# Kernel optimization log

Hardware: AMD Instinct MI355X
Metric: run time of the kernel (lower is better)

Reference implementation:

```python
import jax, jax.numpy as jnp
import numpy as np

N_NODES = 100000


def _sage_conv(x, src, dst, W_l, b_l, W_r):
    # mean-aggregate neighbor (source) features at target nodes
    gathered = x[src]                                   # [E, D]
    summed = jax.ops.segment_sum(gathered, dst, num_segments=N_NODES)  # [N, D]
    deg = jax.ops.segment_sum(jnp.ones((src.shape[0],), x.dtype), dst,
                              num_segments=N_NODES)     # [N]
    mean = summed / jnp.maximum(deg, 1.0)[:, None]      # zero stays zero for isolated nodes
    # PyG SAGEConv: lin_l(aggr) + lin_r(x); bias on lin_l only
    return mean @ W_l + b_l + x @ W_r


def setup_inputs() -> dict:
    key = jax.random.key(0)
    ks = jax.random.split(key, 9)
    x = jax.random.normal(ks[0], (N_NODES, 128), dtype=jnp.float32)
    edge_index = jax.random.randint(ks[1], (2, 1600000), 0, N_NODES, dtype=jnp.int64)
    s1 = 1.0 / np.sqrt(128.0)
    s2 = 1.0 / np.sqrt(32.0)
    return {
        "x": x,
        "edge_index": edge_index,
        "W1_l": jax.random.normal(ks[2], (128, 32), jnp.float32) * s1,
        "b1_l": jax.random.normal(ks[3], (32,), jnp.float32) * s1,
        "W1_r": jax.random.normal(ks[4], (128, 32), jnp.float32) * s1,
        "W2_l": jax.random.normal(ks[5], (32, 32), jnp.float32) * s2,
        "b2_l": jax.random.normal(ks[6], (32,), jnp.float32) * s2,
        "W2_r": jax.random.normal(ks[7], (32, 32), jnp.float32) * s2,
    }


def reference(x, edge_index, W1_l, b1_l, W1_r, W2_l, b2_l, W2_r):
    src, dst = edge_index[0], edge_index[1]
    h = _sage_conv(x, src, dst, W1_l, b1_l, W1_r)
    h = jax.nn.relu(h)
    # dropout is identity in eval mode
    h = _sage_conv(h, src, dst, W2_l, b2_l, W2_r)
    return jax.nn.relu(h)
```

## Files before the change

kernel.cpp:

```cpp
#include <hip/hip_runtime.h>


typedef _Float16 f16;
typedef _Float16 f16x2 __attribute__((ext_vector_type(2)));
typedef _Float16 f16x4 __attribute__((ext_vector_type(4)));
typedef _Float16 half8 __attribute__((ext_vector_type(8)));
typedef float f32x4 __attribute__((ext_vector_type(4)));

#define MAXBINS 2048
#define SHIFT 6
#define BINSZ 64
#define CAP 48
#define BSTR 52
#define GSC 256
#define BSC 512
#define SRC_BITS 17
#define SRC_MASK 0x1FFFFu
#define XSTRIDE 136


__global__ __launch_bounds__(BSC) void block_hist(const int* __restrict__ dst,
                                                  int* __restrict__ blockHist,
                                                  int E, int chunk) {
    __shared__ int sh[MAXBINS];
    for (int i = threadIdx.x; i < MAXBINS; i += BSC) sh[i] = 0;
    __syncthreads();
    int base = blockIdx.x * chunk;
    int end = base + chunk < E ? base + chunk : E;
    for (int e = base + threadIdx.x; e < end; e += BSC)
        atomicAdd(&sh[dst[e] >> SHIFT], 1);
    __syncthreads();
    for (int i = threadIdx.x; i < MAXBINS; i += BSC)
        blockHist[(size_t)blockIdx.x * MAXBINS + i] = sh[i];
}

__global__ __launch_bounds__(256) void col_scan(const int* __restrict__ blockHist,
                                                int* __restrict__ blockBaseRel,
                                                int* __restrict__ binTot) {
    const int wave = threadIdx.x >> 6;
    const int lane = threadIdx.x & 63;
    const int bin = blockIdx.x * 4 + wave;
    int carry = 0;
#pragma unroll
    for (int r = 0; r < GSC / 64; ++r) {
        int b = r * 64 + lane;
        int v = blockHist[(size_t)b * MAXBINS + bin];
        int inc = v;
#pragma unroll
        for (int off = 1; off < 64; off <<= 1) {
            int t = __shfl_up(inc, off, 64);
            if (lane >= off) inc += t;
        }
        blockBaseRel[(size_t)b * MAXBINS + bin] = carry + (inc - v);
        carry += __shfl(inc, 63, 64);
    }
    binTot[bin] = carry;
}

__global__ __launch_bounds__(1024) void scan_bins(const int* __restrict__ binTot,
                                                  int* __restrict__ binStart,
                                                  int* __restrict__ binCnt) {
    __shared__ int sh[1024];
    int t = threadIdx.x;
    int v0 = binTot[2 * t], v1 = binTot[2 * t + 1];
    sh[t] = v0 + v1;
    __syncthreads();
    for (int off = 1; off < 1024; off <<= 1) {
        int x = 0;
        if (t >= off) x = sh[t - off];
        __syncthreads();
        sh[t] += x;
        __syncthreads();
    }
    int excl = sh[t] - (v0 + v1);
    binStart[2 * t] = excl;
    binStart[2 * t + 1] = excl + v0;
    binCnt[2 * t] = v0;
    binCnt[2 * t + 1] = v1;
}

__global__ __launch_bounds__(BSC) void scatter_binned(const int* __restrict__ src,
                                                      const int* __restrict__ dst,
                                                      const int* __restrict__ blockBaseRel,
                                                      const int* __restrict__ binStart,
                                                      unsigned* __restrict__ pairs,
                                                      int E, int chunk) {
    __shared__ int cur[MAXBINS];
    for (int i = threadIdx.x; i < MAXBINS; i += BSC)
        cur[i] = blockBaseRel[(size_t)blockIdx.x * MAXBINS + i] + binStart[i];
    __syncthreads();
    int base = blockIdx.x * chunk;
    int end = base + chunk < E ? base + chunk : E;
    for (int e = base + threadIdx.x; e < end; e += BSC) {
        int s = src[e], d = dst[e];
        int slot = atomicAdd(&cur[d >> SHIFT], 1);
        pairs[slot] = ((unsigned)(d & (BINSZ - 1)) << SRC_BITS) | (unsigned)s;
    }
}


__global__ __launch_bounds__(256) void gemm_mfma(const float* __restrict__ x,
                                                 const float* __restrict__ Wl,
                                                 const float* __restrict__ Wr,
                                                 f16* __restrict__ yl,
                                                 float* __restrict__ yr,
                                                 int N) {
    __shared__ f16 sX[64 * XSTRIDE];
    __shared__ f16 sWT[64 * XSTRIDE];
    const int tid = threadIdx.x;
    const int row0 = blockIdx.x * 64;

    for (int i = tid; i < 64 * 32; i += 256) {
        int r = i >> 5, c4 = i & 31;
        int row = row0 + r;
        float4 v = make_float4(0.f, 0.f, 0.f, 0.f);
        if (row < N) v = *(const float4*)(x + (size_t)row * 128 + c4 * 4);
        f16* d = &sX[r * XSTRIDE + c4 * 4];
        d[0] = (f16)v.x; d[1] = (f16)v.y; d[2] = (f16)v.z; d[3] = (f16)v.w;
    }
    for (int i = tid; i < 64 * 128; i += 256) {
        int k = i >> 6, n = i & 63;
        float v = (n < 32) ? Wl[k * 32 + n] : Wr[k * 32 + (n - 32)];
        sWT[n * XSTRIDE + k] = (f16)v;
    }
    __syncthreads();

    const int w = tid >> 6;
    const int lane = tid & 63;
    const int l15 = lane & 15, quad = lane >> 4;
    f32x4 acc[4] = {};
#pragma unroll
    for (int kc = 0; kc < 4; ++kc) {
        half8 af = *(const half8*)&sX[(w * 16 + l15) * XSTRIDE + kc * 32 + quad * 8];
#pragma unroll
        for (int nt = 0; nt < 4; ++nt) {
            half8 bf = *(const half8*)&sWT[(nt * 16 + l15) * XSTRIDE + kc * 32 + quad * 8];
            acc[nt] = __builtin_amdgcn_mfma_f32_16x16x32_f16(af, bf, acc[nt], 0, 0, 0);
        }
    }
#pragma unroll
    for (int nt = 0; nt < 4; ++nt) {
        int c = nt * 16 + l15;
#pragma unroll
        for (int r = 0; r < 4; ++r) {
            int g = row0 + w * 16 + quad * 4 + r;
            if (c < 32) yl[(size_t)g * 32 + c] = (f16)acc[nt][r];
            else        yr[(size_t)g * 32 + (c - 32)] = acc[nt][r];
        }
    }
}


__global__ __launch_bounds__(256) void agg_l1(const unsigned* __restrict__ pairs,
                                              const int* __restrict__ binStart,
                                              const int* __restrict__ binCnt,
                                              const f16* __restrict__ yl,
                                              const float* __restrict__ yr,
                                              const float* __restrict__ b1,
                                              const float* __restrict__ W2l,
                                              const float* __restrict__ W2r,
                                              f16* __restrict__ zl,
                                              float* __restrict__ zr,
                                              int N) {
    __shared__ __align__(16) int sBucket[BINSZ * BSTR];
    __shared__ int sCnt[BINSZ];
    __shared__ __align__(16) float sW[2048];
    __shared__ __align__(16) float sB[32];
    const int tid = threadIdx.x;
    if (tid < BINSZ) sCnt[tid] = 0;
    if (tid < 32) sB[tid] = b1[tid];
    for (int i = tid; i < 2048; i += 256) sW[i] = (i < 1024) ? W2l[i] : W2r[i - 1024];
    __syncthreads();

    const int b = blockIdx.x;
    const int start = binStart[b];
    const int endE = start + binCnt[b];
    for (int e = start + tid; e < endE; e += 256) {
        unsigned pk = pairs[e];
        int local = pk >> SRC_BITS;
        int slot = atomicAdd(&sCnt[local], 1);
        if (slot < CAP) sBucket[local * BSTR + slot] = (int)(pk & SRC_MASK);
    }
    __syncthreads();

    if (tid < BINSZ) {
        int c = sCnt[tid];
        int m = c < CAP ? c : CAP;
        int mp = (m + 7) & ~7;
        for (int k = m; k < mp; ++k) sBucket[tid * BSTR + k] = N;
    }
    __syncthreads();

    const int node = tid >> 2;
    const int c8 = tid & 3;
    const int node0 = b << SHIFT;
    const int g = node0 + node;

    const int deg = sCnt[node];
    const int m = deg < CAP ? deg : CAP;
    const int q = (m + 7) >> 3;
    const int4* bk = (const int4*)&sBucket[node * BSTR];
    const f16* yb = yl + c8 * 8;

    float ax[8] = {0.f, 0.f, 0.f, 0.f, 0.f, 0.f, 0.f, 0.f};
    for (int j = 0; j < q; ++j) {
        int4 eA = bk[2 * j];
        int4 eB = bk[2 * j + 1];
        half8 v0 = *(const half8*)(yb + (size_t)eA.x * 32);
        half8 v1 = *(const half8*)(yb + (size_t)eA.y * 32);
        half8 v2 = *(const half8*)(yb + (size_t)eA.z * 32);
        half8 v3 = *(const half8*)(yb + (size_t)eA.w * 32);
        half8 w0 = *(const half8*)(yb + (size_t)eB.x * 32);
        half8 w1 = *(const half8*)(yb + (size_t)eB.y * 32);
        half8 w2 = *(const half8*)(yb + (size_t)eB.z * 32);
        half8 w3 = *(const half8*)(yb + (size_t)eB.w * 32);
#pragma unroll
        for (int k = 0; k < 8; ++k)
            ax[k] += (((float)v0[k] + (float)v1[k]) + ((float)v2[k] + (float)v3[k]))
                   + (((float)w0[k] + (float)w1[k]) + ((float)w2[k] + (float)w3[k]));
    }

    float h[8];
    if (g < N) {
        float dg = deg > 1 ? (float)deg : 1.0f;
        float loc[8];
        *(float4*)&loc[0] = *(const float4*)(yr + (size_t)g * 32 + c8 * 8);
        *(float4*)&loc[4] = *(const float4*)(yr + (size_t)g * 32 + c8 * 8 + 4);
#pragma unroll
        for (int k = 0; k < 8; ++k)
            h[k] = fmaxf(ax[k] / dg + sB[c8 * 8 + k] + loc[k], 0.0f);
    } else {
#pragma unroll
        for (int k = 0; k < 8; ++k) h[k] = 0.f;
    }
    __syncthreads();

    float* sH = (float*)sBucket;
    *(float4*)&sH[node * 36 + c8 * 8]     = make_float4(h[0], h[1], h[2], h[3]);
    *(float4*)&sH[node * 36 + c8 * 8 + 4] = make_float4(h[4], h[5], h[6], h[7]);
    __syncthreads();

    const int n2 = tid >> 3;
    const int cq = tid & 7;
    const float4* sW4l = (const float4*)sW;
    const float4* sW4r = (const float4*)(sW + 1024);
#pragma unroll
    for (int it = 0; it < 2; ++it) {
        int n = it * 32 + n2;
        int gg = node0 + n;
        float4 al = make_float4(0.f, 0.f, 0.f, 0.f);
        float4 ar = make_float4(0.f, 0.f, 0.f, 0.f);
#pragma unroll 8
        for (int k = 0; k < 32; ++k) {
            float hk = sH[n * 36 + k];
            float4 wl = sW4l[k * 8 + cq];
            float4 wr = sW4r[k * 8 + cq];
            al.x += hk * wl.x; al.y += hk * wl.y; al.z += hk * wl.z; al.w += hk * wl.w;
            ar.x += hk * wr.x; ar.y += hk * wr.y; ar.z += hk * wr.z; ar.w += hk * wr.w;
        }
        f16x4 hh;
        hh[0] = (f16)al.x; hh[1] = (f16)al.y; hh[2] = (f16)al.z; hh[3] = (f16)al.w;
        *(f16x4*)(zl + (size_t)gg * 32 + cq * 4) = hh;
        if (gg < N) *(float4*)(zr + (size_t)gg * 32 + cq * 4) = ar;
    }
}

__global__ __launch_bounds__(256) void agg_l2(const unsigned* __restrict__ pairs,
                                              const int* __restrict__ binStart,
                                              const int* __restrict__ binCnt,
                                              const f16* __restrict__ zl,
                                              const float* __restrict__ b2,
                                              float* __restrict__ io,
                                              int N) {
    __shared__ __align__(16) int sBucket[BINSZ * BSTR];
    __shared__ int sCnt[BINSZ];
    __shared__ __align__(16) float sB[32];
    const int tid = threadIdx.x;
    if (tid < BINSZ) sCnt[tid] = 0;
    if (tid < 32) sB[tid] = b2[tid];
    __syncthreads();

    const int b = blockIdx.x;
    const int start = binStart[b];
    const int endE = start + binCnt[b];
    for (int e = start + tid; e < endE; e += 256) {
        unsigned pk = pairs[e];
        int local = pk >> SRC_BITS;
        int slot = atomicAdd(&sCnt[local], 1);
        if (slot < CAP) sBucket[local * BSTR + slot] = (int)(pk & SRC_MASK);
    }
    __syncthreads();

    if (tid < BINSZ) {
        int c = sCnt[tid];
        int m = c < CAP ? c : CAP;
        int mp = (m + 7) & ~7;
        for (int k = m; k < mp; ++k) sBucket[tid * BSTR + k] = N;
    }
    __syncthreads();

    const int node = tid >> 2;
    const int c8 = tid & 3;
    const int node0 = b << SHIFT;
    const int g = node0 + node;

    const int deg = sCnt[node];
    const int m = deg < CAP ? deg : CAP;
    const int q = (m + 7) >> 3;
    const int4* bk = (const int4*)&sBucket[node * BSTR];
    const f16* zb = zl + c8 * 8;

    float ax[8] = {0.f, 0.f, 0.f, 0.f, 0.f, 0.f, 0.f, 0.f};
    for (int j = 0; j < q; ++j) {
        int4 eA = bk[2 * j];
        int4 eB = bk[2 * j + 1];
        half8 v0 = *(const half8*)(zb + (size_t)eA.x * 32);
        half8 v1 = *(const half8*)(zb + (size_t)eA.y * 32);
        half8 v2 = *(const half8*)(zb + (size_t)eA.z * 32);
        half8 v3 = *(const half8*)(zb + (size_t)eA.w * 32);
        half8 w0 = *(const half8*)(zb + (size_t)eB.x * 32);
        half8 w1 = *(const half8*)(zb + (size_t)eB.y * 32);
        half8 w2 = *(const half8*)(zb + (size_t)eB.z * 32);
        half8 w3 = *(const half8*)(zb + (size_t)eB.w * 32);
#pragma unroll
        for (int k = 0; k < 8; ++k)
            ax[k] += (((float)v0[k] + (float)v1[k]) + ((float)v2[k] + (float)v3[k]))
                   + (((float)w0[k] + (float)w1[k]) + ((float)w2[k] + (float)w3[k]));
    }

    if (g < N) {
        float dg = deg > 1 ? (float)deg : 1.0f;
        float v[8];
        *(float4*)&v[0] = *(const float4*)(io + (size_t)g * 32 + c8 * 8);
        *(float4*)&v[4] = *(const float4*)(io + (size_t)g * 32 + c8 * 8 + 4);
        float o[8];
#pragma unroll
        for (int k = 0; k < 8; ++k)
            o[k] = fmaxf(ax[k] / dg + sB[c8 * 8 + k] + v[k], 0.0f);
        *(float4*)(io + (size_t)g * 32 + c8 * 8)     = *(float4*)&o[0];
        *(float4*)(io + (size_t)g * 32 + c8 * 8 + 4) = *(float4*)&o[4];
    }
}

extern "C" void kernel_launch(void* const* d_in, const int* in_sizes, int n_in,
                              void* d_out, int out_size, void* d_ws, size_t ws_size,
                              hipStream_t stream) {
    const float* x    = (const float*)d_in[0];
    const int*   ei   = (const int*)d_in[1];
    const float* W1l  = (const float*)d_in[2];
    const float* b1l  = (const float*)d_in[3];
    const float* W1r  = (const float*)d_in[4];
    const float* W2l  = (const float*)d_in[5];
    const float* b2l  = (const float*)d_in[6];
    const float* W2r  = (const float*)d_in[7];

    const int N = in_sizes[0] / 128;
    const int E = in_sizes[1] / 2;
    const int* srcIdx = ei;
    const int* dstIdx = ei + E;

    const int gridG = (N >> 6) + 1;
    const int NP = gridG << 6;

    const int nbins = (N + BINSZ - 1) >> SHIFT;
    const int chunk = (E + GSC - 1) / GSC;

    int*      blockHist = (int*)d_ws;
    int*      blockBase = blockHist + (size_t)GSC * MAXBINS;
    int*      binTot    = blockBase + (size_t)GSC * MAXBINS;
    int*      binStart  = binTot + MAXBINS;
    int*      binCnt    = binStart + MAXBINS;
    unsigned* pairs     = (unsigned*)(binCnt + MAXBINS);
    f16*      A         = (f16*)(pairs + E);
    float*    B         = (float*)(A + (size_t)NP * 32);
    f16*      Z         = (f16*)(B + (size_t)NP * 32);
    float*    outp      = (float*)d_out;

    block_hist<<<GSC, BSC, 0, stream>>>(dstIdx, blockHist, E, chunk);
    col_scan<<<MAXBINS / 4, 256, 0, stream>>>(blockHist, blockBase, binTot);
    scan_bins<<<1, 1024, 0, stream>>>(binTot, binStart, binCnt);
    scatter_binned<<<GSC, BSC, 0, stream>>>(srcIdx, dstIdx, blockBase, binStart,
                                            pairs, E, chunk);

    gemm_mfma<<<gridG, 256, 0, stream>>>(x, W1l, W1r, A, B, N);
    agg_l1<<<nbins, 256, 0, stream>>>(pairs, binStart, binCnt, A, B, b1l,
                                      W2l, W2r, Z, outp, N);
    agg_l2<<<nbins, 256, 0, stream>>>(pairs, binStart, binCnt, Z, b2l, outp, N);
}
```

Before: 201.6 us.

## Fuse histogram into GEMM launch and use fixed-capacity bins without global scan

Merges the dst-histogram blocks and the first-layer MFMA GEMM into one launch. It also drops the bin-total scan kernel by giving each bin a fixed 2048-slot region in the pairs buffer, so each bin starts at bin<<11 and only per-block offsets are needed. Edge loads in the histogram, scatter and aggregation kernels are vectorised to int4/uint4, and bucket padding is pre-filled instead of patched after the fill. The fixed per-bin capacity assumes no 64-node bin receives more than 2048 edges. That holds for uniformly random graphs but would overflow for skewed ones.

Result: no change. 198.9 us (-1.3%).

```diff
diff --git a/kernel.cpp b/kernel.cpp
--- a/kernel.cpp
+++ b/kernel.cpp
@@ -12,6 +12,7 @@
 #define BINSZ 64
 #define CAP 48
 #define BSTR 52
+#define BC_SHIFT 11
 #define GSC 256
 #define BSC 512
 #define SRC_BITS 17
@@ -19,95 +20,45 @@
 #define XSTRIDE 136
 
 
-__global__ __launch_bounds__(BSC) void block_hist(const int* __restrict__ dst,
-                                                  int* __restrict__ blockHist,
-                                                  int E, int chunk) {
-    __shared__ int sh[MAXBINS];
-    for (int i = threadIdx.x; i < MAXBINS; i += BSC) sh[i] = 0;
-    __syncthreads();
-    int base = blockIdx.x * chunk;
-    int end = base + chunk < E ? base + chunk : E;
-    for (int e = base + threadIdx.x; e < end; e += BSC)
-        atomicAdd(&sh[dst[e] >> SHIFT], 1);
-    __syncthreads();
-    for (int i = threadIdx.x; i < MAXBINS; i += BSC)
-        blockHist[(size_t)blockIdx.x * MAXBINS + i] = sh[i];
-}
-
-__global__ __launch_bounds__(256) void col_scan(const int* __restrict__ blockHist,
-                                                int* __restrict__ blockBaseRel,
-                                                int* __restrict__ binTot) {
-    const int wave = threadIdx.x >> 6;
-    const int lane = threadIdx.x & 63;
-    const int bin = blockIdx.x * 4 + wave;
-    int carry = 0;
-#pragma unroll
-    for (int r = 0; r < GSC / 64; ++r) {
-        int b = r * 64 + lane;
-        int v = blockHist[(size_t)b * MAXBINS + bin];
-        int inc = v;
-#pragma unroll
-        for (int off = 1; off < 64; off <<= 1) {
-            int t = __shfl_up(inc, off, 64);
-            if (lane >= off) inc += t;
-        }
-        blockBaseRel[(size_t)b * MAXBINS + bin] = carry + (inc - v);
-        carry += __shfl(inc, 63, 64);
-    }
-    binTot[bin] = carry;
-}
-
-__global__ __launch_bounds__(1024) void scan_bins(const int* __restrict__ binTot,
-                                                  int* __restrict__ binStart,
-                                                  int* __restrict__ binCnt) {
-    __shared__ int sh[1024];
-    int t = threadIdx.x;
-    int v0 = binTot[2 * t], v1 = binTot[2 * t + 1];
-    sh[t] = v0 + v1;
-    __syncthreads();
-    for (int off = 1; off < 1024; off <<= 1) {
-        int x = 0;
-        if (t >= off) x = sh[t - off];
+__global__ __launch_bounds__(256) void prep(const float* __restrict__ x,
+                                            const float* __restrict__ Wl,
+                                            const float* __restrict__ Wr,
+                                            const int* __restrict__ dstIdx,
+                                            int* __restrict__ blockHist,
+                                            f16* __restrict__ yl,
+                                            float* __restrict__ yr,
+                                            int N, int E, int chunk, int gridG) {
+    __shared__ __align__(16) f16 smem[2 * 64 * XSTRIDE];
+    const int tid = threadIdx.x;
+
+    if ((int)blockIdx.x >= gridG) {
+        int* sh = (int*)smem;
+        for (int i = tid; i < MAXBINS; i += 256) sh[i] = 0;
         __syncthreads();
-        sh[t] += x;
+        const int hb = blockIdx.x - gridG;
+        const int base = hb * chunk;
+        const int end = base + chunk < E ? base + chunk : E;
+        if (base < E) {
+            const int nv = (end - base) >> 2;
+            const int4* d4 = (const int4*)(dstIdx + base);
+            for (int i = tid; i < nv; i += 256) {
+                int4 d = d4[i];
+                atomicAdd(&sh[d.x >> SHIFT], 1);
+                atomicAdd(&sh[d.y >> SHIFT], 1);
+                atomicAdd(&sh[d.z >> SHIFT], 1);
+                atomicAdd(&sh[d.w >> SHIFT], 1);
+            }
+            const int rem = (end - base) & 3;
+            if (tid < rem) atomicAdd(&sh[dstIdx[base + nv * 4 + tid] >> SHIFT], 1);
+        }
         __syncthreads();
-    }
-    int excl = sh[t] - (v0 + v1);
-    binStart[2 * t] = excl;
-    binStart[2 * t + 1] = excl + v0;
-    binCnt[2 * t] = v0;
-    binCnt[2 * t + 1] = v1;
-}
-
-__global__ __launch_bounds__(BSC) void scatter_binned(const int* __restrict__ src,
-                                                      const int* __restrict__ dst,
-                                                      const int* __restrict__ blockBaseRel,
-                                                      const int* __restrict__ binStart,
-                                                      unsigned* __restrict__ pairs,
-                                                      int E, int chunk) {
-    __shared__ int cur[MAXBINS];
-    for (int i = threadIdx.x; i < MAXBINS; i += BSC)
-        cur[i] = blockBaseRel[(size_t)blockIdx.x * MAXBINS + i] + binStart[i];
-    __syncthreads();
-    int base = blockIdx.x * chunk;
-    int end = base + chunk < E ? base + chunk : E;
-    for (int e = base + threadIdx.x; e < end; e += BSC) {
-        int s = src[e], d = dst[e];
-        int slot = atomicAdd(&cur[d >> SHIFT], 1);
-        pairs[slot] = ((unsigned)(d & (BINSZ - 1)) << SRC_BITS) | (unsigned)s;
-    }
-}
-
-
-__global__ __launch_bounds__(256) void gemm_mfma(const float* __restrict__ x,
-                                                 const float* __restrict__ Wl,
-                                                 const float* __restrict__ Wr,
-                                                 f16* __restrict__ yl,
-                                                 float* __restrict__ yr,
-                                                 int N) {
-    __shared__ f16 sX[64 * XSTRIDE];
-    __shared__ f16 sWT[64 * XSTRIDE];
-    const int tid = threadIdx.x;
+        for (int i = tid; i < MAXBINS; i += 256)
+            blockHist[(size_t)hb * MAXBINS + i] = sh[i];
+        return;
+    }
+
+    f16* sX = smem;
+    f16* sWT = smem + 64 * XSTRIDE;
     const int row0 = blockIdx.x * 64;
 
     for (int i = tid; i < 64 * 32; i += 256) {
@@ -150,9 +101,68 @@
     }
 }
 
+__global__ __launch_bounds__(256) void col_scan(const int* __restrict__ blockHist,
+                                                int* __restrict__ blockBaseRel,
+                                                int* __restrict__ binCnt) {
+    const int wave = threadIdx.x >> 6;
+    const int lane = threadIdx.x & 63;
+    const int bin = blockIdx.x * 4 + wave;
+    int carry = 0;
+#pragma unroll
+    for (int r = 0; r < GSC / 64; ++r) {
+        int b = r * 64 + lane;
+        int v = blockHist[(size_t)b * MAXBINS + bin];
+        int inc = v;
+#pragma unroll
+        for (int off = 1; off < 64; off <<= 1) {
+            int t = __shfl_up(inc, off, 64);
+            if (lane >= off) inc += t;
+        }
+        blockBaseRel[(size_t)b * MAXBINS + bin] = carry + (inc - v);
+        carry += __shfl(inc, 63, 64);
+    }
+    binCnt[bin] = carry;
+}
+
+__global__ __launch_bounds__(BSC) void scatter_binned(const int* __restrict__ src,
+                                                      const int* __restrict__ dst,
+                                                      const int* __restrict__ blockBaseRel,
+                                                      unsigned* __restrict__ pairs,
+                                                      int E, int chunk) {
+    __shared__ int cur[MAXBINS];
+    for (int i = threadIdx.x; i < MAXBINS; i += BSC)
+        cur[i] = blockBaseRel[(size_t)blockIdx.x * MAXBINS + i] + (i << BC_SHIFT);
+    __syncthreads();
+    const int base = blockIdx.x * chunk;
+    const int end = base + chunk < E ? base + chunk : E;
+    if (base >= E) return;
+    const int nv = (end - base) >> 2;
+    const int4* s4 = (const int4*)(src + base);
+    const int4* d4 = (const int4*)(dst + base);
+    for (int i = threadIdx.x; i < nv; i += BSC) {
+        int4 s = s4[i];
+        int4 d = d4[i];
+        int slot;
+        slot = atomicAdd(&cur[d.x >> SHIFT], 1);
+        pairs[slot] = ((unsigned)(d.x & (BINSZ - 1)) << SRC_BITS) | (unsigned)s.x;
+        slot = atomicAdd(&cur[d.y >> SHIFT], 1);
+        pairs[slot] = ((unsigned)(d.y & (BINSZ - 1)) << SRC_BITS) | (unsigned)s.y;
+        slot = atomicAdd(&cur[d.z >> SHIFT], 1);
+        pairs[slot] = ((unsigned)(d.z & (BINSZ - 1)) << SRC_BITS) | (unsigned)s.z;
+        slot = atomicAdd(&cur[d.w >> SHIFT], 1);
+        pairs[slot] = ((unsigned)(d.w & (BINSZ - 1)) << SRC_BITS) | (unsigned)s.w;
+    }
+    const int rem = (end - base) & 3;
+    if ((int)threadIdx.x < rem) {
+        int e = base + nv * 4 + threadIdx.x;
+        int s = src[e], d = dst[e];
+        int slot = atomicAdd(&cur[d >> SHIFT], 1);
+        pairs[slot] = ((unsigned)(d & (BINSZ - 1)) << SRC_BITS) | (unsigned)s;
+    }
+}
+
 
 __global__ __launch_bounds__(256) void agg_l1(const unsigned* __restrict__ pairs,
-                                              const int* __restrict__ binStart,
                                               const int* __restrict__ binCnt,
                                               const f16* __restrict__ yl,
                                               const float* __restrict__ yr,
@@ -169,25 +179,39 @@
     const int tid = threadIdx.x;
     if (tid < BINSZ) sCnt[tid] = 0;
     if (tid < 32) sB[tid] = b1[tid];
-    for (int i = tid; i < 2048; i += 256) sW[i] = (i < 1024) ? W2l[i] : W2r[i - 1024];
+    {
+        float4* sW4 = (float4*)sW;
+        sW4[tid] = ((const float4*)W2l)[tid];
+        sW4[256 + tid] = ((const float4*)W2r)[tid];
+        for (int i = tid; i < BINSZ * BSTR; i += 256) sBucket[i] = N;
+    }
     __syncthreads();
 
     const int b = blockIdx.x;
-    const int start = binStart[b];
-    const int endE = start + binCnt[b];
-    for (int e = start + tid; e < endE; e += 256) {
-        unsigned pk = pairs[e];
-        int local = pk >> SRC_BITS;
-        int slot = atomicAdd(&sCnt[local], 1);
-        if (slot < CAP) sBucket[local * BSTR + slot] = (int)(pk & SRC_MASK);
-    }
-    __syncthreads();
-
-    if (tid < BINSZ) {
-        int c = sCnt[tid];
-        int m = c < CAP ? c : CAP;
-        int mp = (m + 7) & ~7;
-        for (int k = m; k < mp; ++k) sBucket[tid * BSTR + k] = N;
+    const unsigned* pb = pairs + ((size_t)b << BC_SHIFT);
+    const int cnt = binCnt[b];
+    const int nv = cnt >> 2;
+    const uint4* p4 = (const uint4*)pb;
+    for (int i = tid; i < nv; i += 256) {
+        uint4 pk = p4[i];
+        int l, s;
+        l = pk.x >> SRC_BITS; s = atomicAdd(&sCnt[l], 1);
+        if (s < CAP) sBucket[l * BSTR + s] = (int)(pk.x & SRC_MASK);
+        l = pk.y >> SRC_BITS; s = atomicAdd(&sCnt[l], 1);
+        if (s < CAP) sBucket[l * BSTR + s] = (int)(pk.y & SRC_MASK);
+        l = pk.z >> SRC_BITS; s = atomicAdd(&sCnt[l], 1);
+        if (s < CAP) sBucket[l * BSTR + s] = (int)(pk.z & SRC_MASK);
+        l = pk.w >> SRC_BITS; s = atomicAdd(&sCnt[l], 1);
+        if (s < CAP) sBucket[l * BSTR + s] = (int)(pk.w & SRC_MASK);
+    }
+    {
+        const int rem = cnt & 3;
+        if (tid < rem) {
+            unsigned pk = pb[nv * 4 + tid];
+            int l = pk >> SRC_BITS;
+            int s = atomicAdd(&sCnt[l], 1);
+            if (s < CAP) sBucket[l * BSTR + s] = (int)(pk & SRC_MASK);
+        }
     }
     __syncthreads();
 
@@ -266,7 +290,6 @@
 }
 
 __global__ __launch_bounds__(256) void agg_l2(const unsigned* __restrict__ pairs,
-                                              const int* __restrict__ binStart,
                                               const int* __restrict__ binCnt,
                                               const f16* __restrict__ zl,
                                               const float* __restrict__ b2,
@@ -278,24 +301,34 @@
     const int tid = threadIdx.x;
     if (tid < BINSZ) sCnt[tid] = 0;
     if (tid < 32) sB[tid] = b2[tid];
+    for (int i = tid; i < BINSZ * BSTR; i += 256) sBucket[i] = N;
     __syncthreads();
 
     const int b = blockIdx.x;
-    const int start = binStart[b];
-    const int endE = start + binCnt[b];
-    for (int e = start + tid; e < endE; e += 256) {
-        unsigned pk = pairs[e];
-        int local = pk >> SRC_BITS;
-        int slot = atomicAdd(&sCnt[local], 1);
-        if (slot < CAP) sBucket[local * BSTR + slot] = (int)(pk & SRC_MASK);
-    }
-    __syncthreads();
-
-    if (tid < BINSZ) {
-        int c = sCnt[tid];
-        int m = c < CAP ? c : CAP;
-        int mp = (m + 7) & ~7;
-        for (int k = m; k < mp; ++k) sBucket[tid * BSTR + k] = N;
+    const unsigned* pb = pairs + ((size_t)b << BC_SHIFT);
+    const int cnt = binCnt[b];
+    const int nv = cnt >> 2;
+    const uint4* p4 = (const uint4*)pb;
+    for (int i = tid; i < nv; i += 256) {
+        uint4 pk = p4[i];
+        int l, s;
+        l = pk.x >> SRC_BITS; s = atomicAdd(&sCnt[l], 1);
+        if (s < CAP) sBucket[l * BSTR + s] = (int)(pk.x & SRC_MASK);
+        l = pk.y >> SRC_BITS; s = atomicAdd(&sCnt[l], 1);
+        if (s < CAP) sBucket[l * BSTR + s] = (int)(pk.y & SRC_MASK);
+        l = pk.z >> SRC_BITS; s = atomicAdd(&sCnt[l], 1);
+        if (s < CAP) sBucket[l * BSTR + s] = (int)(pk.z & SRC_MASK);
+        l = pk.w >> SRC_BITS; s = atomicAdd(&sCnt[l], 1);
+        if (s < CAP) sBucket[l * BSTR + s] = (int)(pk.w & SRC_MASK);
+    }
+    {
+        const int rem = cnt & 3;
+        if (tid < rem) {
+            unsigned pk = pb[nv * 4 + tid];
+            int l = pk >> SRC_BITS;
+            int s = atomicAdd(&sCnt[l], 1);
+            if (s < CAP) sBucket[l * BSTR + s] = (int)(pk & SRC_MASK);
+        }
     }
     __syncthreads();
 
@@ -363,27 +396,23 @@
     const int NP = gridG << 6;
 
     const int nbins = (N + BINSZ - 1) >> SHIFT;
-    const int chunk = (E + GSC - 1) / GSC;
+    const int chunk = (((E + GSC - 1) / GSC) + 3) & ~3;
 
     int*      blockHist = (int*)d_ws;
     int*      blockBase = blockHist + (size_t)GSC * MAXBINS;
-    int*      binTot    = blockBase + (size_t)GSC * MAXBINS;
-    int*      binStart  = binTot + MAXBINS;
-    int*      binCnt    = binStart + MAXBINS;
+    int*      binCnt    = blockBase + (size_t)GSC * MAXBINS;
     unsigned* pairs     = (unsigned*)(binCnt + MAXBINS);
-    f16*      A         = (f16*)(pairs + E);
+    f16*      A         = (f16*)(pairs + ((size_t)MAXBINS << BC_SHIFT));
     float*    B         = (float*)(A + (size_t)NP * 32);
     f16*      Z         = (f16*)(B + (size_t)NP * 32);
     float*    outp      = (float*)d_out;
 
-    block_hist<<<GSC, BSC, 0, stream>>>(dstIdx, blockHist, E, chunk);
-    col_scan<<<MAXBINS / 4, 256, 0, stream>>>(blockHist, blockBase, binTot);
-    scan_bins<<<1, 1024, 0, stream>>>(binTot, binStart, binCnt);
-    scatter_binned<<<GSC, BSC, 0, stream>>>(srcIdx, dstIdx, blockBase, binStart,
+    prep<<<gridG + GSC, 256, 0, stream>>>(x, W1l, W1r, dstIdx, blockHist,
+                                          A, B, N, E, chunk, gridG);
+    col_scan<<<MAXBINS / 4, 256, 0, stream>>>(blockHist, blockBase, binCnt);
+    scatter_binned<<<GSC, BSC, 0, stream>>>(srcIdx, dstIdx, blockBase,
                                             pairs, E, chunk);
-
-    gemm_mfma<<<gridG, 256, 0, stream>>>(x, W1l, W1r, A, B, N);
-    agg_l1<<<nbins, 256, 0, stream>>>(pairs, binStart, binCnt, A, B, b1l,
+    agg_l1<<<nbins, 256, 0, stream>>>(pairs, binCnt, A, B, b1l,
                                       W2l, W2r, Z, outp, N);
-    agg_l2<<<nbins, 256, 0, stream>>>(pairs, binStart, binCnt, Z, b2l, outp, N);
-}
+    agg_l2<<<nbins, 256, 0, stream>>>(pairs, binCnt, Z, b2l, outp, N);
+}
```

## Replace global bin sort with per-block local sort and segment descriptors

Applied to the files above, without the earlier changes.

The four-kernel global counting sort (histogram, column scan, bin scan, scatter) becomes a single scatter_sort kernel. Each block sorts its own edge chunk by destination bin into a private region and writes a packed offset/count descriptor per (bin, block). The aggregation kernels then gather their bin's edges from all 256 block segments through these descriptors, and pre-fill the bucket with the sentinel instead of padding afterwards. This removes three launches and the global scan traffic, but each aggregation block now does 256 scattered small reads. It also assumes the edge arrays are 16-byte aligned, uses int4 loads, and packs offsets into 16 bits.

Measured after the change: 194.8 us. 3.4% less time.

```diff
diff --git a/kernel.cpp b/kernel.cpp
--- a/kernel.cpp
+++ b/kernel.cpp
@@ -19,94 +19,14 @@
 #define XSTRIDE 136
 
 
-__global__ __launch_bounds__(BSC) void block_hist(const int* __restrict__ dst,
-                                                  int* __restrict__ blockHist,
-                                                  int E, int chunk) {
-    __shared__ int sh[MAXBINS];
-    for (int i = threadIdx.x; i < MAXBINS; i += BSC) sh[i] = 0;
-    __syncthreads();
-    int base = blockIdx.x * chunk;
-    int end = base + chunk < E ? base + chunk : E;
-    for (int e = base + threadIdx.x; e < end; e += BSC)
-        atomicAdd(&sh[dst[e] >> SHIFT], 1);
-    __syncthreads();
-    for (int i = threadIdx.x; i < MAXBINS; i += BSC)
-        blockHist[(size_t)blockIdx.x * MAXBINS + i] = sh[i];
-}
-
-__global__ __launch_bounds__(256) void col_scan(const int* __restrict__ blockHist,
-                                                int* __restrict__ blockBaseRel,
-                                                int* __restrict__ binTot) {
-    const int wave = threadIdx.x >> 6;
-    const int lane = threadIdx.x & 63;
-    const int bin = blockIdx.x * 4 + wave;
-    int carry = 0;
-#pragma unroll
-    for (int r = 0; r < GSC / 64; ++r) {
-        int b = r * 64 + lane;
-        int v = blockHist[(size_t)b * MAXBINS + bin];
-        int inc = v;
-#pragma unroll
-        for (int off = 1; off < 64; off <<= 1) {
-            int t = __shfl_up(inc, off, 64);
-            if (lane >= off) inc += t;
-        }
-        blockBaseRel[(size_t)b * MAXBINS + bin] = carry + (inc - v);
-        carry += __shfl(inc, 63, 64);
-    }
-    binTot[bin] = carry;
-}
-
-__global__ __launch_bounds__(1024) void scan_bins(const int* __restrict__ binTot,
-                                                  int* __restrict__ binStart,
-                                                  int* __restrict__ binCnt) {
-    __shared__ int sh[1024];
-    int t = threadIdx.x;
-    int v0 = binTot[2 * t], v1 = binTot[2 * t + 1];
-    sh[t] = v0 + v1;
-    __syncthreads();
-    for (int off = 1; off < 1024; off <<= 1) {
-        int x = 0;
-        if (t >= off) x = sh[t - off];
-        __syncthreads();
-        sh[t] += x;
-        __syncthreads();
-    }
-    int excl = sh[t] - (v0 + v1);
-    binStart[2 * t] = excl;
-    binStart[2 * t + 1] = excl + v0;
-    binCnt[2 * t] = v0;
-    binCnt[2 * t + 1] = v1;
-}
-
-__global__ __launch_bounds__(BSC) void scatter_binned(const int* __restrict__ src,
-                                                      const int* __restrict__ dst,
-                                                      const int* __restrict__ blockBaseRel,
-                                                      const int* __restrict__ binStart,
-                                                      unsigned* __restrict__ pairs,
-                                                      int E, int chunk) {
-    __shared__ int cur[MAXBINS];
-    for (int i = threadIdx.x; i < MAXBINS; i += BSC)
-        cur[i] = blockBaseRel[(size_t)blockIdx.x * MAXBINS + i] + binStart[i];
-    __syncthreads();
-    int base = blockIdx.x * chunk;
-    int end = base + chunk < E ? base + chunk : E;
-    for (int e = base + threadIdx.x; e < end; e += BSC) {
-        int s = src[e], d = dst[e];
-        int slot = atomicAdd(&cur[d >> SHIFT], 1);
-        pairs[slot] = ((unsigned)(d & (BINSZ - 1)) << SRC_BITS) | (unsigned)s;
-    }
-}
-
-
 __global__ __launch_bounds__(256) void gemm_mfma(const float* __restrict__ x,
                                                  const float* __restrict__ Wl,
                                                  const float* __restrict__ Wr,
                                                  f16* __restrict__ yl,
                                                  float* __restrict__ yr,
                                                  int N) {
-    __shared__ f16 sX[64 * XSTRIDE];
-    __shared__ f16 sWT[64 * XSTRIDE];
+    __shared__ __align__(16) f16 sX[64 * XSTRIDE];
+    __shared__ __align__(16) f16 sWT[64 * XSTRIDE];
     const int tid = threadIdx.x;
     const int row0 = blockIdx.x * 64;
 
@@ -151,9 +71,120 @@
 }
 
 
+__global__ __launch_bounds__(BSC) void scatter_sort(const int* __restrict__ src,
+                                                    const int* __restrict__ dst,
+                                                    unsigned* __restrict__ pairs,
+                                                    unsigned* __restrict__ binSeg,
+                                                    int E, int chunk) {
+    __shared__ int cnt[MAXBINS];
+    __shared__ int wsum[8];
+    const int tid = threadIdx.x;
+    const int sb = blockIdx.x;
+    for (int i = tid; i < MAXBINS; i += BSC) cnt[i] = 0;
+    __syncthreads();
+
+    const int base = sb * chunk;
+    const int endE = base + chunk < E ? base + chunk : E;
+    const int len = endE > base ? endE - base : 0;
+    const int nv = len >> 2;
+    const int rem = len & 3;
+    const int4* s4 = (const int4*)(src + base);
+    const int4* d4 = (const int4*)(dst + base);
+
+    for (int i = tid; i < nv; i += BSC) {
+        int4 d = d4[i];
+        atomicAdd(&cnt[d.x >> SHIFT], 1);
+        atomicAdd(&cnt[d.y >> SHIFT], 1);
+        atomicAdd(&cnt[d.z >> SHIFT], 1);
+        atomicAdd(&cnt[d.w >> SHIFT], 1);
+    }
+    if (tid < rem) atomicAdd(&cnt[dst[base + nv * 4 + tid] >> SHIFT], 1);
+    __syncthreads();
+
+    {
+        int b0 = cnt[4 * tid], b1 = cnt[4 * tid + 1],
+            b2 = cnt[4 * tid + 2], b3 = cnt[4 * tid + 3];
+        int tsum = b0 + b1 + b2 + b3;
+        const int lane = tid & 63, wave = tid >> 6;
+        int incl = tsum;
+#pragma unroll
+        for (int off = 1; off < 64; off <<= 1) {
+            int t = __shfl_up(incl, off, 64);
+            if (lane >= off) incl += t;
+        }
+        if (lane == 63) wsum[wave] = incl;
+        __syncthreads();
+        if (tid == 0) {
+            int a = 0;
+#pragma unroll
+            for (int w = 0; w < 8; ++w) { int t = wsum[w]; wsum[w] = a; a += t; }
+        }
+        __syncthreads();
+        int ex = (incl - tsum) + wsum[wave];
+        int e0 = ex, e1 = ex + b0, e2 = e1 + b1, e3 = e2 + b2;
+        binSeg[(size_t)(4 * tid) * GSC + sb]     = ((unsigned)e0 << 16) | (unsigned)b0;
+        binSeg[(size_t)(4 * tid + 1) * GSC + sb] = ((unsigned)e1 << 16) | (unsigned)b1;
+        binSeg[(size_t)(4 * tid + 2) * GSC + sb] = ((unsigned)e2 << 16) | (unsigned)b2;
+        binSeg[(size_t)(4 * tid + 3) * GSC + sb] = ((unsigned)e3 << 16) | (unsigned)b3;
+        __syncthreads();
+        cnt[4 * tid] = e0; cnt[4 * tid + 1] = e1;
+        cnt[4 * tid + 2] = e2; cnt[4 * tid + 3] = e3;
+    }
+    __syncthreads();
+
+    unsigned* out = pairs + (size_t)sb * chunk;
+    for (int i = tid; i < nv; i += BSC) {
+        int4 s = s4[i];
+        int4 d = d4[i];
+        int slot;
+        slot = atomicAdd(&cnt[d.x >> SHIFT], 1);
+        out[slot] = ((unsigned)(d.x & (BINSZ - 1)) << SRC_BITS) | (unsigned)s.x;
+        slot = atomicAdd(&cnt[d.y >> SHIFT], 1);
+        out[slot] = ((unsigned)(d.y & (BINSZ - 1)) << SRC_BITS) | (unsigned)s.y;
+        slot = atomicAdd(&cnt[d.z >> SHIFT], 1);
+        out[slot] = ((unsigned)(d.z & (BINSZ - 1)) << SRC_BITS) | (unsigned)s.z;
+        slot = atomicAdd(&cnt[d.w >> SHIFT], 1);
+        out[slot] = ((unsigned)(d.w & (BINSZ - 1)) << SRC_BITS) | (unsigned)s.w;
+    }
+    if (tid < rem) {
+        int e = base + nv * 4 + tid;
+        int s = src[e], d = dst[e];
+        int slot = atomicAdd(&cnt[d >> SHIFT], 1);
+        out[slot] = ((unsigned)(d & (BINSZ - 1)) << SRC_BITS) | (unsigned)s;
+    }
+}
+
+
+__device__ __forceinline__ void build_bucket(const unsigned* __restrict__ pairs,
+                                             const unsigned* __restrict__ binSeg,
+                                             int* sBucket, int* sCnt,
+                                             int b, int tid, int chunk) {
+    unsigned dsc = binSeg[(size_t)b * GSC + tid];
+    int scnt = (int)(dsc & 0xFFFFu);
+    const unsigned* p = pairs + (size_t)tid * chunk + (dsc >> 16);
+    int k = 0;
+    for (; k + 4 <= scnt; k += 4) {
+        unsigned p0 = p[k], p1 = p[k + 1], p2 = p[k + 2], p3 = p[k + 3];
+        int l, s;
+        l = p0 >> SRC_BITS; s = atomicAdd(&sCnt[l], 1);
+        if (s < CAP) sBucket[l * BSTR + s] = (int)(p0 & SRC_MASK);
+        l = p1 >> SRC_BITS; s = atomicAdd(&sCnt[l], 1);
+        if (s < CAP) sBucket[l * BSTR + s] = (int)(p1 & SRC_MASK);
+        l = p2 >> SRC_BITS; s = atomicAdd(&sCnt[l], 1);
+        if (s < CAP) sBucket[l * BSTR + s] = (int)(p2 & SRC_MASK);
+        l = p3 >> SRC_BITS; s = atomicAdd(&sCnt[l], 1);
+        if (s < CAP) sBucket[l * BSTR + s] = (int)(p3 & SRC_MASK);
+    }
+    for (; k < scnt; ++k) {
+        unsigned pk = p[k];
+        int l = pk >> SRC_BITS;
+        int s = atomicAdd(&sCnt[l], 1);
+        if (s < CAP) sBucket[l * BSTR + s] = (int)(pk & SRC_MASK);
+    }
+}
+
 __global__ __launch_bounds__(256) void agg_l1(const unsigned* __restrict__ pairs,
-                                              const int* __restrict__ binStart,
-                                              const int* __restrict__ binCnt,
+                                              const unsigned* __restrict__ binSeg,
                                               const f16* __restrict__ yl,
                                               const float* __restrict__ yr,
                                               const float* __restrict__ b1,
@@ -161,7 +192,7 @@
                                               const float* __restrict__ W2r,
                                               f16* __restrict__ zl,
                                               float* __restrict__ zr,
-                                              int N) {
+                                              int N, int chunk) {
     __shared__ __align__(16) int sBucket[BINSZ * BSTR];
     __shared__ int sCnt[BINSZ];
     __shared__ __align__(16) float sW[2048];
@@ -169,26 +200,16 @@
     const int tid = threadIdx.x;
     if (tid < BINSZ) sCnt[tid] = 0;
     if (tid < 32) sB[tid] = b1[tid];
-    for (int i = tid; i < 2048; i += 256) sW[i] = (i < 1024) ? W2l[i] : W2r[i - 1024];
+    {
+        float4* sW4 = (float4*)sW;
+        sW4[tid] = ((const float4*)W2l)[tid];
+        sW4[256 + tid] = ((const float4*)W2r)[tid];
+        for (int i = tid; i < BINSZ * BSTR; i += 256) sBucket[i] = N;
+    }
     __syncthreads();
 
     const int b = blockIdx.x;
-    const int start = binStart[b];
-    const int endE = start + binCnt[b];
-    for (int e = start + tid; e < endE; e += 256) {
-        unsigned pk = pairs[e];
-        int local = pk >> SRC_BITS;
-        int slot = atomicAdd(&sCnt[local], 1);
-        if (slot < CAP) sBucket[local * BSTR + slot] = (int)(pk & SRC_MASK);
-    }
-    __syncthreads();
-
-    if (tid < BINSZ) {
-        int c = sCnt[tid];
-        int m = c < CAP ? c : CAP;
-        int mp = (m + 7) & ~7;
-        for (int k = m; k < mp; ++k) sBucket[tid * BSTR + k] = N;
-    }
+    build_bucket(pairs, binSeg, sBucket, sCnt, b, tid, chunk);
     __syncthreads();
 
     const int node = tid >> 2;
@@ -266,37 +287,22 @@
 }
 
 __global__ __launch_bounds__(256) void agg_l2(const unsigned* __restrict__ pairs,
-                                              const int* __restrict__ binStart,
-                                              const int* __restrict__ binCnt,
+                                              const unsigned* __restrict__ binSeg,
                                               const f16* __restrict__ zl,
                                               const float* __restrict__ b2,
                                               float* __restrict__ io,
-                                              int N) {
+                                              int N, int chunk) {
     __shared__ __align__(16) int sBucket[BINSZ * BSTR];
     __shared__ int sCnt[BINSZ];
     __shared__ __align__(16) float sB[32];
     const int tid = threadIdx.x;
     if (tid < BINSZ) sCnt[tid] = 0;
     if (tid < 32) sB[tid] = b2[tid];
+    for (int i = tid; i < BINSZ * BSTR; i += 256) sBucket[i] = N;
     __syncthreads();
 
     const int b = blockIdx.x;
-    const int start = binStart[b];
-    const int endE = start + binCnt[b];
-    for (int e = start + tid; e < endE; e += 256) {
-        unsigned pk = pairs[e];
-        int local = pk >> SRC_BITS;
-        int slot = atomicAdd(&sCnt[local], 1);
-        if (slot < CAP) sBucket[local * BSTR + slot] = (int)(pk & SRC_MASK);
-    }
-    __syncthreads();
-
-    if (tid < BINSZ) {
-        int c = sCnt[tid];
-        int m = c < CAP ? c : CAP;
-        int mp = (m + 7) & ~7;
-        for (int k = m; k < mp; ++k) sBucket[tid * BSTR + k] = N;
-    }
+    build_bucket(pairs, binSeg, sBucket, sCnt, b, tid, chunk);
     __syncthreads();
 
     const int node = tid >> 2;
@@ -363,27 +369,18 @@
     const int NP = gridG << 6;
 
     const int nbins = (N + BINSZ - 1) >> SHIFT;
-    const int chunk = (E + GSC - 1) / GSC;
-
-    int*      blockHist = (int*)d_ws;
-    int*      blockBase = blockHist + (size_t)GSC * MAXBINS;
-    int*      binTot    = blockBase + (size_t)GSC * MAXBINS;
-    int*      binStart  = binTot + MAXBINS;
-    int*      binCnt    = binStart + MAXBINS;
-    unsigned* pairs     = (unsigned*)(binCnt + MAXBINS);
-    f16*      A         = (f16*)(pairs + E);
-    float*    B         = (float*)(A + (size_t)NP * 32);
-    f16*      Z         = (f16*)(B + (size_t)NP * 32);
-    float*    outp      = (float*)d_out;
-
-    block_hist<<<GSC, BSC, 0, stream>>>(dstIdx, blockHist, E, chunk);
-    col_scan<<<MAXBINS / 4, 256, 0, stream>>>(blockHist, blockBase, binTot);
-    scan_bins<<<1, 1024, 0, stream>>>(binTot, binStart, binCnt);
-    scatter_binned<<<GSC, BSC, 0, stream>>>(srcIdx, dstIdx, blockBase, binStart,
-                                            pairs, E, chunk);
+    const int chunk = (((E + GSC - 1) / GSC) + 3) & ~3;
+
+    unsigned* binSeg = (unsigned*)d_ws;
+    unsigned* pairs  = binSeg + (size_t)MAXBINS * GSC;
+    f16*      A      = (f16*)(pairs + (size_t)GSC * chunk);
+    float*    B      = (float*)(A + (size_t)NP * 32);
+    f16*      Z      = (f16*)(B + (size_t)NP * 32);
+    float*    outp   = (float*)d_out;
 
     gemm_mfma<<<gridG, 256, 0, stream>>>(x, W1l, W1r, A, B, N);
-    agg_l1<<<nbins, 256, 0, stream>>>(pairs, binStart, binCnt, A, B, b1l,
-                                      W2l, W2r, Z, outp, N);
-    agg_l2<<<nbins, 256, 0, stream>>>(pairs, binStart, binCnt, Z, b2l, outp, N);
-}
+    scatter_sort<<<GSC, BSC, 0, stream>>>(srcIdx, dstIdx, pairs, binSeg, E, chunk);
+    agg_l1<<<nbins, 256, 0, stream>>>(pairs, binSeg, A, B, b1l,
+                                      W2l, W2r, Z, outp, N, chunk);
+    agg_l2<<<nbins, 256, 0, stream>>>(pairs, binSeg, Z, b2l, outp, N, chunk);
+}
```
